# Kernel tuning notes

Measured on AMD Instinct MI355X. Metric: run time of the kernel, lower is better.

## Reference

```python
import jax, jax.numpy as jnp
import numpy as np
from jax import lax

D_MODEL = 512
N_BLOCKS = 8
VOCAB = 2048
MEL = 80
D_INNER = 2 * D_MODEL      # standard Mamba expand=2
STATE = 16                 # AudioConstants.MAMBA_STATE_DIM
DT_RANK = D_MODEL // 16    # 32
CONV_K = 4                 # causal depthwise conv kernel
B, T = 4, 2048


def setup_inputs() -> dict:
    key = jax.random.key(0)
    ks = jax.random.split(key, 16)
    s = 0.02
    nb = N_BLOCKS
    inp = {
        "feats": jax.random.normal(ks[0], (B, T, MEL), jnp.float32),
        "feat_lens": jax.random.randint(ks[1], (B,), 0, T, jnp.int32),
        # frontend
        "conv1_w": jax.random.normal(ks[2], (D_MODEL, MEL, 3), jnp.float32) * s,
        "conv1_b": jnp.zeros((D_MODEL,), jnp.float32),
        "conv2_w": jax.random.normal(ks[3], (D_MODEL, D_MODEL, 3), jnp.float32) * s,
        "conv2_b": jnp.zeros((D_MODEL,), jnp.float32),
        # stacked per-block Mamba params (leading dim = n_blocks)
        "norm_w": jnp.ones((nb, D_MODEL), jnp.float32),
        "in_proj_w": jax.random.normal(ks[4], (nb, D_MODEL, 2 * D_INNER), jnp.float32) * s,
        "dwconv_w": jax.random.normal(ks[5], (nb, D_INNER, CONV_K), jnp.float32) * s,
        "dwconv_b": jnp.zeros((nb, D_INNER), jnp.float32),
        "x_proj_w": jax.random.normal(ks[6], (nb, D_INNER, DT_RANK + 2 * STATE), jnp.float32) * s,
        "dt_proj_w": jax.random.normal(ks[7], (nb, DT_RANK, D_INNER), jnp.float32) * s,
        "dt_proj_b": jnp.full((nb, D_INNER), -4.6, jnp.float32),  # softplus(-4.6)~0.01
        "A_log": jnp.tile(jnp.log(jnp.arange(1, STATE + 1, dtype=jnp.float32))[None, None, :], (nb, D_INNER, 1)),
        "Dskip": jnp.ones((nb, D_INNER), jnp.float32),
        "out_proj_w": jax.random.normal(ks[8], (nb, D_INNER, D_MODEL), jnp.float32) * s,
        # CTC head
        "head_w": jax.random.normal(ks[9], (D_MODEL, VOCAB), jnp.float32) * s,
        "head_b": jnp.zeros((VOCAB,), jnp.float32),
    }
    return inp


def _conv1d(x, w, b, stride, pad):
    # x: (B, Cin, L), w: (Cout, Cin, K)
    y = lax.conv_general_dilated(x, w, (stride,), [(pad, pad)],
                                 dimension_numbers=("NCH", "OIH", "NCH"))
    return y + b[None, :, None]


def _mamba_layer(x, p):
    nw, ipw, cw, cb, xpw, dpw, dpb, alog, dsk, opw = p
    res = x
    # RMSNorm
    xn = x * lax.rsqrt(jnp.mean(x * x, axis=-1, keepdims=True) + 1e-5) * nw
    xz = xn @ ipw                                # (B, L, 2*di)
    xs, z = jnp.split(xz, 2, axis=-1)
    # causal depthwise conv over time
    xc = jnp.pad(xs.transpose(0, 2, 1), ((0, 0), (0, 0), (CONV_K - 1, 0)))
    xc = lax.conv_general_dilated(xc, cw[:, None, :], (1,), [(0, 0)],
                                  dimension_numbers=("NCH", "OIH", "NCH"),
                                  feature_group_count=D_INNER)
    xs = jax.nn.silu((xc + cb[None, :, None]).transpose(0, 2, 1))  # (B, L, di)
    # input-dependent SSM params
    xdb = xs @ xpw                               # (B, L, dt_rank + 2N)
    dt, Bm, Cm = jnp.split(xdb, [DT_RANK, DT_RANK + STATE], axis=-1)
    delta = jax.nn.softplus(dt @ dpw + dpb)      # (B, L, di)
    A = -jnp.exp(alog)                           # (di, N)
    dA = jnp.exp(delta[..., None] * A)           # (B, L, di, N)
    dBx = delta[..., None] * Bm[:, :, None, :] * xs[..., None]

    def step(h, inp):
        dA_t, dBx_t, C_t = inp                   # (B,di,N),(B,di,N),(B,N)
        h = dA_t * h + dBx_t
        y = jnp.einsum("bdn,bn->bd", h, C_t)
        return h, y

    h0 = jnp.zeros((x.shape[0], D_INNER, STATE), x.dtype)
    _, ys = lax.scan(step, h0, (dA.transpose(1, 0, 2, 3),
                                dBx.transpose(1, 0, 2, 3),
                                Cm.transpose(1, 0, 2)))
    y = ys.transpose(1, 0, 2) + xs * dsk          # (B, L, di)
    y = y * jax.nn.silu(z)
    return res + y @ opw, None


def reference(feats, feat_lens, conv1_w, conv1_b, conv2_w, conv2_b,
              norm_w, in_proj_w, dwconv_w, dwconv_b, x_proj_w,
              dt_proj_w, dt_proj_b, A_log, Dskip, out_proj_w,
              head_w, head_b):
    x = feats.transpose(0, 2, 1)                  # (B, 80, T)
    x = jax.nn.gelu(_conv1d(x, conv1_w, conv1_b, 2, 1), approximate=False)
    x = jax.nn.gelu(_conv1d(x, conv2_w, conv2_b, 2, 1), approximate=False)
    x = x.transpose(0, 2, 1)                      # (B, T/4, D)
    params = (norm_w, in_proj_w, dwconv_w, dwconv_b, x_proj_w,
              dt_proj_w, dt_proj_b, A_log, Dskip, out_proj_w)
    x, _ = lax.scan(_mamba_layer, x, params)
    logits = x @ head_w + head_b                  # (B, T/4, V)
    out_lens = jnp.maximum(feat_lens // 4, 1)
    return logits, out_lens
```

## Files before the change

kernel.cpp:

```cpp
#include <hip/hip_runtime.h>
#include <hip/hip_bf16.h>

#define DMODEL 512
#define NB 8
#define VOCABSZ 2048
#define MEL 80
#define DIN 1024
#define NSTATE 16
#define DTRANK 32
#define BATCH 4
#define TIN 2048
#define LL1 1024
#define LSEQ 512
#define MROWS (BATCH*LSEQ)
#define M1ROWS (BATCH*LL1)
#define NCHUNK 16
#define LCHUNK 32

typedef unsigned short u16;
typedef unsigned int   u32;
typedef __attribute__((ext_vector_type(8))) short short8;
typedef __attribute__((ext_vector_type(4))) float f32x4;

__device__ __forceinline__ float bf2f(u16 v) { return __uint_as_float(((u32)v) << 16); }
__device__ __forceinline__ u16 f2bf(float f) {
    u32 u = __float_as_uint(f);
    return (u16)((u + 0x7fffu + ((u >> 16) & 1u)) >> 16);
}
__device__ __forceinline__ float gelu_exact(float v) {
    return 0.5f * v * (1.0f + erff(v * 0.70710678118654752f));
}
__device__ __forceinline__ float silu_f(float v) { return v / (1.0f + __expf(-v)); }
__device__ __forceinline__ float softplus_f(float v) { return v > 20.f ? v : log1pf(__expf(v)); }

template<int WM, int WN, int MR, int NR, int EPI, int SPLITK>
__global__ __launch_bounds__(WM*WN*64) void gemm2_bf16(
    const u16* __restrict__ A, int lda,
    const u16* __restrict__ BT, int ldb,
    const float* __restrict__ bias,
    float* __restrict__ Cf, u16* __restrict__ Cb, int ldc,
    int K, int zstride)
{
    constexpr int BM = WM * MR * 16;
    constexpr int BN = WN * NR * 16;
    constexpr int NT = WM * WN * 64;
    constexpr int LA = (BM * 4) / NT;
    constexpr int LB = (BN * 4) / NT;
    __shared__ __align__(16) u16 As[2][BM * 32];
    __shared__ __align__(16) u16 Bs[2][BN * 32];
    const int tid = threadIdx.x;
    const int m0 = blockIdx.y * BM, n0 = blockIdx.x * BN;
    const int lane = tid & 63;
    const int wave = tid >> 6;
    const int wm = wave / WN, wn = wave % WN;
    const int lr = lane & 15, lk = lane >> 4;

    int kt0 = 0, kend = K;
    if (SPLITK > 1) {
        const int kb = K / SPLITK;
        kt0 = blockIdx.z * kb;
        kend = kt0 + kb;
        Cf += (size_t)blockIdx.z * zstride;
    }

    f32x4 acc[MR][NR];
#pragma unroll
    for (int m = 0; m < MR; ++m)
#pragma unroll
        for (int n = 0; n < NR; ++n) acc[m][n] = (f32x4){0.f, 0.f, 0.f, 0.f};

    auto stage = [&](int buf, int kt) {
#pragma unroll
        for (int c = 0; c < LA; ++c) {
            int idx = c * NT + tid;
            const u16* src = A + (size_t)(m0 + (idx >> 2)) * lda + kt + (idx & 3) * 8;
            __builtin_amdgcn_global_load_lds(
                (const __attribute__((address_space(1))) void*)src,
                (__attribute__((address_space(3))) void*)&As[buf][idx * 8], 16, 0, 0);
        }
#pragma unroll
        for (int c = 0; c < LB; ++c) {
            int idx = c * NT + tid;
            const u16* src = BT + (size_t)(n0 + (idx >> 2)) * ldb + kt + (idx & 3) * 8;
            __builtin_amdgcn_global_load_lds(
                (const __attribute__((address_space(1))) void*)src,
                (__attribute__((address_space(3))) void*)&Bs[buf][idx * 8], 16, 0, 0);
        }
    };

    stage(0, kt0);
    __syncthreads();
    int cur = 0;
    for (int kt = kt0; kt < kend; kt += 32) {
        if (kt + 32 < kend) stage(cur ^ 1, kt + 32);
        short8 a[MR], b[NR];
#pragma unroll
        for (int m = 0; m < MR; ++m)
            a[m] = *(const short8*)&As[cur][((wm * MR + m) * 16 + lr) * 32 + lk * 8];
#pragma unroll
        for (int n = 0; n < NR; ++n)
            b[n] = *(const short8*)&Bs[cur][((wn * NR + n) * 16 + lr) * 32 + lk * 8];
#pragma unroll
        for (int m = 0; m < MR; ++m)
#pragma unroll
            for (int n = 0; n < NR; ++n)
                acc[m][n] = __builtin_amdgcn_mfma_f32_16x16x32_bf16(a[m], b[n], acc[m][n], 0, 0, 0);
        __syncthreads();
        cur ^= 1;
    }

#pragma unroll
    for (int m = 0; m < MR; ++m) {
#pragma unroll
        for (int n = 0; n < NR; ++n) {
#pragma unroll
            for (int r = 0; r < 4; ++r) {
                const int row = m0 + (wm * MR + m) * 16 + lk * 4 + r;
                const int col = n0 + (wn * NR + n) * 16 + lr;
                float v = acc[m][n][r];
                if (EPI == 1)      v += bias[col];
                else if (EPI == 2) v = gelu_exact(v + bias[col]);
                else if (EPI == 3) v = softplus_f(v + bias[col]);
                else if (EPI == 4) v += Cf[(size_t)row * ldc + col];
                if (Cf) Cf[(size_t)row * ldc + col] = v;
                if (Cb) Cb[(size_t)row * ldc + col] = f2bf(v);
            }
        }
    }
}

__global__ __launch_bounds__(256) void tcast_k(const float* __restrict__ in, u16* __restrict__ out,
                                               int R, int C, size_t sin, size_t sout) {
    in  += (size_t)blockIdx.z * sin;
    out += (size_t)blockIdx.z * sout;
    __shared__ float s[32][33];
    const int tx = threadIdx.x & 31, ty = threadIdx.x >> 5;
    const int r0 = blockIdx.y * 32, c0 = blockIdx.x * 32;
#pragma unroll
    for (int i = 0; i < 4; ++i)
        s[ty + i * 8][tx] = in[(size_t)(r0 + ty + i * 8) * C + c0 + tx];
    __syncthreads();
#pragma unroll
    for (int i = 0; i < 4; ++i)
        out[(size_t)(c0 + ty + i * 8) * R + r0 + tx] = f2bf(s[tx][ty + i * 8]);
}

__global__ void castpad_k(const float* __restrict__ in, u16* __restrict__ out,
                          int rows, int cin, int cout, int instride,
                          size_t sin, size_t sout) {
    in  += (size_t)blockIdx.z * sin;
    out += (size_t)blockIdx.z * sout;
    int idx = blockIdx.x * 256 + threadIdx.x;
    if (idx >= rows * cout) return;
    int c = idx % cout, r = idx / cout;
    out[idx] = (c < cin) ? f2bf(in[(size_t)r * instride + c]) : (u16)0;
}

__global__ void im2col1_k(const float* __restrict__ feats, u16* __restrict__ out) {
    int idx = blockIdx.x * 256 + threadIdx.x;
    int c = idx & 255, m = idx >> 8;
    int l1 = m & (LL1 - 1), b = m >> 10;
    float v = 0.f;
    if (c < 240) {
        int ci = c / 3, kk = c - ci * 3;
        int t = 2 * l1 - 1 + kk;
        if (t >= 0 && t < TIN) v = feats[((size_t)b * TIN + t) * MEL + ci];
    }
    out[idx] = f2bf(v);
}

__global__ void im2col2_k(const float* __restrict__ y1, u16* __restrict__ out) {
    int idx = blockIdx.x * 256 + threadIdx.x;
    int c = idx % 1536, m = idx / 1536;
    int l = m & (LSEQ - 1), b = m >> 9;
    int ci = c / 3, kk = c - ci * 3;
    int t = 2 * l - 1 + kk;
    float v = (t >= 0 && t < LL1) ? y1[((size_t)b * LL1 + t) * 512 + ci] : 0.f;
    out[idx] = f2bf(v);
}

__global__ __launch_bounds__(256) void rmsnorm_k(const float* __restrict__ x,
                                                 const float* __restrict__ nw,
                                                 u16* __restrict__ xn) {
    int m = blockIdx.x;
    int tid = threadIdx.x;
    const float2 v = *reinterpret_cast<const float2*>(&x[(size_t)m * DMODEL + tid * 2]);
    float ss = v.x * v.x + v.y * v.y;
#pragma unroll
    for (int o = 32; o > 0; o >>= 1) ss += __shfl_down(ss, o);
    __shared__ float sred[4];
    __shared__ float sscale;
    if ((tid & 63) == 0) sred[tid >> 6] = ss;
    __syncthreads();
    if (tid == 0) {
        float tot = sred[0] + sred[1] + sred[2] + sred[3];
        sscale = rsqrtf(tot / 512.f + 1e-5f);
    }
    __syncthreads();
    float sc = sscale;
    u32 pack = (u32)f2bf(v.x * sc * nw[tid * 2]) | ((u32)f2bf(v.y * sc * nw[tid * 2 + 1]) << 16);
    *reinterpret_cast<u32*>(&xn[(size_t)m * DMODEL + tid * 2]) = pack;
}

__global__ __launch_bounds__(256) void dwconv_silu_k(const u16* __restrict__ xzb,
                                                     const float* __restrict__ cw,
                                                     const float* __restrict__ cb,
                                                     float* __restrict__ xs,
                                                     u16* __restrict__ xsb) {
    int d = blockIdx.x * 256 + threadIdx.x;
    int m = blockIdx.y;
    int l = m & (LSEQ - 1);
    int b = m >> 9;
    float acc = cb[d];
    const float4 w4 = *reinterpret_cast<const float4*>(&cw[d * 4]);
    const float wk[4] = {w4.x, w4.y, w4.z, w4.w};
#pragma unroll
    for (int k = 0; k < 4; k++) {
        int t = l - 3 + k;
        if (t >= 0) acc += wk[k] * bf2f(xzb[((size_t)(b * LSEQ + t)) * (2 * DIN) + d]);
    }
    float o = silu_f(acc);
    xs[(size_t)m * DIN + d] = o;
    xsb[(size_t)m * DIN + d] = f2bf(o);
}

__global__ void xreduce_k(const float* __restrict__ part, float* __restrict__ xdb,
                          u16* __restrict__ dtb) {
    int idx = blockIdx.x * 256 + threadIdx.x;
    float s = part[idx] + part[131072 + idx] + part[262144 + idx] + part[393216 + idx];
    xdb[idx] = s;
    int c = idx & 63, r = idx >> 6;
    if (c < 32) dtb[r * 32 + c] = f2bf(s);
}

template<int PASS>
__global__ __launch_bounds__(256) void scan_chunk_k(
    const u16* __restrict__ deltab, const float* __restrict__ xs,
    const float* __restrict__ xdb, const u16* __restrict__ xzb,
    const float* __restrict__ alog, const float* __restrict__ dsk,
    const float* __restrict__ hin,
    float* __restrict__ Pout, float* __restrict__ Qout,
    u16* __restrict__ yb)
{
    __shared__ float s_bc[LCHUNK * 32];
    __shared__ float s_dl[LCHUNK * 64];
    __shared__ float s_xs[LCHUNK * 64];
    __shared__ float s_z [PASS ? LCHUNK * 64 : 1];

    const int tid  = threadIdx.x;
    const int j    = tid & 3;
    const int dsub = tid >> 2;
    const int d0   = blockIdx.x * 64;
    const int c    = blockIdx.y;
    const int b    = blockIdx.z;
    const int d    = d0 + dsub;
    const size_t rbase = (size_t)b * LSEQ + c * LCHUNK;

    for (int idx = tid; idx < LCHUNK * 32; idx += 256) {
        int t = idx >> 5, cc = idx & 31;
        s_bc[idx] = xdb[(rbase + t) * 64 + 32 + cc];
    }
    for (int idx = tid; idx < LCHUNK * 64; idx += 256) {
        int t = idx >> 6, dd = idx & 63;
        s_dl[idx] = bf2f(deltab[(rbase + t) * DIN + d0 + dd]);
        s_xs[idx] = xs[(rbase + t) * DIN + d0 + dd];
        if (PASS) s_z[idx] = bf2f(xzb[(rbase + t) * (2 * DIN) + DIN + d0 + dd]);
    }
    __syncthreads();

    float a[4], h[4];
#pragma unroll
    for (int nj = 0; nj < 4; nj++)
        a[nj] = -__expf(alog[(size_t)d * NSTATE + j * 4 + nj]);

    const size_t chbase = ((size_t)(b * NCHUNK + c) * DIN + d) * NSTATE + j * 4;
    if (PASS) {
        const float4 h4 = *reinterpret_cast<const float4*>(&hin[chbase]);
        h[0] = h4.x; h[1] = h4.y; h[2] = h4.z; h[3] = h4.w;
    } else {
        h[0] = h[1] = h[2] = h[3] = 0.f;
    }
    const float dskv = PASS ? dsk[d] : 0.f;
    float sdl = 0.f;

    for (int t = 0; t < LCHUNK; t++) {
        const float dl = s_dl[t * 64 + dsub];
        const float xv = s_xs[t * 64 + dsub];
        const float dlx = dl * xv;
        if (!PASS) sdl += dl;
        float yv = 0.f;
#pragma unroll
        for (int nj = 0; nj < 4; nj++) {
            const float bn = s_bc[t * 32 + j * 4 + nj];
            const float dA = __expf(dl * a[nj]);
            h[nj] = fmaf(dA, h[nj], dlx * bn);
            if (PASS) {
                const float cn = s_bc[t * 32 + 16 + j * 4 + nj];
                yv = fmaf(h[nj], cn, yv);
            }
        }
        if (PASS) {
            yv += __shfl_xor(yv, 1);
            yv += __shfl_xor(yv, 2);
            if (j == 0) {
                const float zv = s_z[t * 64 + dsub];
                yb[(rbase + t) * DIN + d] = f2bf((yv + xv * dskv) * silu_f(zv));
            }
        }
    }

    if (!PASS) {
        float4 Pv, Qv;
        Pv.x = __expf(a[0] * sdl); Pv.y = __expf(a[1] * sdl);
        Pv.z = __expf(a[2] * sdl); Pv.w = __expf(a[3] * sdl);
        Qv.x = h[0]; Qv.y = h[1]; Qv.z = h[2]; Qv.w = h[3];
        *reinterpret_cast<float4*>(&Pout[chbase]) = Pv;
        *reinterpret_cast<float4*>(&Qout[chbase]) = Qv;
    }
}

__global__ __launch_bounds__(256) void scan_mid_k(const float* __restrict__ P,
                                                  float* __restrict__ Q) {
    const int tid = blockIdx.x * 256 + threadIdx.x;
    const int b  = tid >> 14;
    const int dn = tid & 16383;
    const size_t base = (size_t)b * (NCHUNK * DIN * NSTATE) + dn;
    float p[NCHUNK], q[NCHUNK];
#pragma unroll
    for (int c = 0; c < NCHUNK; c++) {
        p[c] = P[base + (size_t)c * (DIN * NSTATE)];
        q[c] = Q[base + (size_t)c * (DIN * NSTATE)];
    }
    float h = 0.f;
    Q[base] = 0.f;
#pragma unroll
    for (int c = 1; c < NCHUNK; c++) {
        h = fmaf(p[c - 1], h, q[c - 1]);
        Q[base + (size_t)c * (DIN * NSTATE)] = h;
    }
}

__global__ void lens_k(const int* __restrict__ feat_lens, float* __restrict__ out) {
    int b = threadIdx.x;
    if (b < BATCH) {
        int v = feat_lens[b] / 4;
        if (v < 1) v = 1;
        out[b] = (float)v;
    }
}

extern "C" void kernel_launch(void* const* d_in, const int* in_sizes, int n_in,
                              void* d_out, int out_size, void* d_ws, size_t ws_size,
                              hipStream_t stream)
{
    const float* feats = (const float*)d_in[0];
    const int*   flens = (const int*)  d_in[1];
    const float* c1w = (const float*)d_in[2];
    const float* c1b = (const float*)d_in[3];
    const float* c2w = (const float*)d_in[4];
    const float* c2b = (const float*)d_in[5];
    const float* nw  = (const float*)d_in[6];
    const float* ipw = (const float*)d_in[7];
    const float* cw  = (const float*)d_in[8];
    const float* cb  = (const float*)d_in[9];
    const float* xpw = (const float*)d_in[10];
    const float* dpw = (const float*)d_in[11];
    const float* dpb = (const float*)d_in[12];
    const float* alog= (const float*)d_in[13];
    const float* dskp= (const float*)d_in[14];
    const float* opw = (const float*)d_in[15];
    const float* hw  = (const float*)d_in[16];
    const float* hb  = (const float*)d_in[17];

    float* ws = (float*)d_ws;
    u16*  XZb   = (u16*)ws;
    float* X    = ws + 2097152;
    u16*  XN    = (u16*)(ws + 3145728);
    u16*  Xb    = (u16*)(ws + 3670016);
    float* XS   = ws + 4194304;
    u16*  XSb   = (u16*)(ws + 6291456);
    u16*  DELb  = (u16*)(ws + 7340032);
    float* XDB  = ws + 8388608;
    float* P    = ws + 8519680;
    u16*  dtb   = (u16*)(ws + 9568256);
    u16*  Yb    = (u16*)(ws + 9633792);
    float* XDBp = ws + 10682368;
    u16*  ipwT  = (u16*)(ws + 11206656);
    u16*  opwT  = (u16*)(ws + 11730944);
    u16*  hwT   = (u16*)(ws + 11993088);
    u16*  xpwT  = (u16*)(ws + 12517376);
    u16*  dpwT  = (u16*)(ws + 12779520);
    u16*  c1wb  = (u16*)(ws + 12910592);
    u16*  c2wb  = (u16*)(ws + 12976128);
    float* Y1   = XS;
    float* logits = (float*)d_out;
    float* Q    = logits;

    castpad_k<<<dim3(512, 1, 1), 256, 0, stream>>>(c1w, c1wb, 512, 240, 256, 240, 0, 0);
    castpad_k<<<dim3(3072, 1, 1), 256, 0, stream>>>(c2w, c2wb, 512, 1536, 1536, 1536, 0, 0);
    tcast_k<<<dim3(64, 16, 1), 256, 0, stream>>>(hw, hwT, 512, 2048, 0, 0);
    tcast_k<<<dim3(2, 32, 8), 256, 0, stream>>>(xpw, xpwT, 1024, 64, 65536, 65536);
    tcast_k<<<dim3(32, 1, 8), 256, 0, stream>>>(dpw, dpwT, 32, 1024, 32768, 32768);

    im2col1_k<<<4096, 256, 0, stream>>>(feats, XZb);
    gemm2_bf16<2, 2, 4, 2, 2, 1><<<dim3(8, 32), 256, 0, stream>>>(
        XZb, 256, c1wb, 256, c1b, Y1, nullptr, 512, 256, 0);
    im2col2_k<<<12288, 256, 0, stream>>>(Y1, XZb);
    gemm2_bf16<2, 2, 2, 2, 2, 1><<<dim3(8, 32), 256, 0, stream>>>(
        XZb, 1536, c2wb, 1536, c2b, X, nullptr, 512, 1536, 0);

    for (int blk = 0; blk < NB; ++blk) {
        tcast_k<<<dim3(64, 16, 1), 256, 0, stream>>>(ipw + (size_t)blk * 1048576, ipwT, 512, 2048, 0, 0);
        tcast_k<<<dim3(16, 32, 1), 256, 0, stream>>>(opw + (size_t)blk * 524288, opwT, 1024, 512, 0, 0);
        rmsnorm_k<<<MROWS, 256, 0, stream>>>(X, nw + blk * DMODEL, XN);
        gemm2_bf16<2, 2, 4, 2, 0, 1><<<dim3(32, 16), 256, 0, stream>>>(
            XN, 512, ipwT, 512, nullptr, nullptr, XZb, 2048, 512, 0);
        dwconv_silu_k<<<dim3(4, MROWS), 256, 0, stream>>>(
            XZb, cw + blk * DIN * 4, cb + blk * DIN, XS, XSb);
        gemm2_bf16<2, 2, 2, 2, 0, 4><<<dim3(1, 32, 4), 256, 0, stream>>>(
            XSb, 1024, xpwT + (size_t)blk * 65536, 1024, nullptr,
            XDBp, nullptr, 64, 1024, 131072);
        xreduce_k<<<512, 256, 0, stream>>>(XDBp, XDB, dtb);
        gemm2_bf16<2, 2, 4, 2, 3, 1><<<dim3(16, 16), 256, 0, stream>>>(
            dtb, 32, dpwT + (size_t)blk * 32768, 32, dpb + blk * DIN,
            nullptr, DELb, 1024, 32, 0);
        scan_chunk_k<0><<<dim3(16, NCHUNK, BATCH), 256, 0, stream>>>(
            DELb, XS, XDB, nullptr, alog + (size_t)blk * DIN * NSTATE,
            nullptr, nullptr, P, Q, nullptr);
        scan_mid_k<<<256, 256, 0, stream>>>(P, Q);
        scan_chunk_k<1><<<dim3(16, NCHUNK, BATCH), 256, 0, stream>>>(
            DELb, XS, XDB, XZb, alog + (size_t)blk * DIN * NSTATE,
            dskp + blk * DIN, Q, nullptr, nullptr, Yb);
        gemm2_bf16<2, 2, 2, 2, 4, 1><<<dim3(8, 32), 256, 0, stream>>>(
            Yb, 1024, opwT, 1024, nullptr, X, Xb, 512, 1024, 0);
    }

    gemm2_bf16<2, 2, 4, 2, 1, 1><<<dim3(32, 16), 256, 0, stream>>>(
        Xb, 512, hwT, 512, hb, logits, nullptr, 2048, 512, 0);
    lens_k<<<1, 64, 0, stream>>>(flens, logits + (size_t)MROWS * VOCABSZ);
}
```

Measured before the change: 884.7 us.

## Hoist weight casts, drop fp32 activations, fold chunk-carry scan into second pass

Moves the per-block in_proj and out_proj transpose-cast kernels out of the layer loop into one batched launch each. The conv1 output and the dwconv output are now stored only as bf16, which removes the fp32 XS buffer and its writes and reads. The xreduce kernel is vectorised with float4 loads and packed stores. The separate scan_mid kernel is removed; each second-pass scan block now rebuilds its carry-in state by walking the previous chunks' P/Q. This saves one launch per layer but adds redundant serial work that grows with the chunk index, and storing xs in bf16 lowers scan precision.

```diff
diff --git a/kernel.cpp b/kernel.cpp
--- a/kernel.cpp
+++ b/kernel.cpp
@@ -169,14 +169,13 @@
     out[idx] = f2bf(v);
 }
 
-__global__ void im2col2_k(const float* __restrict__ y1, u16* __restrict__ out) {
+__global__ void im2col2_k(const u16* __restrict__ y1b, u16* __restrict__ out) {
     int idx = blockIdx.x * 256 + threadIdx.x;
     int c = idx % 1536, m = idx / 1536;
     int l = m & (LSEQ - 1), b = m >> 9;
     int ci = c / 3, kk = c - ci * 3;
     int t = 2 * l - 1 + kk;
-    float v = (t >= 0 && t < LL1) ? y1[((size_t)b * LL1 + t) * 512 + ci] : 0.f;
-    out[idx] = f2bf(v);
+    out[idx] = (t >= 0 && t < LL1) ? y1b[((size_t)b * LL1 + t) * 512 + ci] : (u16)0;
 }
 
 __global__ __launch_bounds__(256) void rmsnorm_k(const float* __restrict__ x,
@@ -205,7 +204,6 @@
 __global__ __launch_bounds__(256) void dwconv_silu_k(const u16* __restrict__ xzb,
                                                      const float* __restrict__ cw,
                                                      const float* __restrict__ cb,
-                                                     float* __restrict__ xs,
                                                      u16* __restrict__ xsb) {
     int d = blockIdx.x * 256 + threadIdx.x;
     int m = blockIdx.y;
@@ -219,27 +217,37 @@
         int t = l - 3 + k;
         if (t >= 0) acc += wk[k] * bf2f(xzb[((size_t)(b * LSEQ + t)) * (2 * DIN) + d]);
     }
-    float o = silu_f(acc);
-    xs[(size_t)m * DIN + d] = o;
-    xsb[(size_t)m * DIN + d] = f2bf(o);
+    xsb[(size_t)m * DIN + d] = f2bf(silu_f(acc));
 }
 
 __global__ void xreduce_k(const float* __restrict__ part, float* __restrict__ xdb,
                           u16* __restrict__ dtb) {
-    int idx = blockIdx.x * 256 + threadIdx.x;
-    float s = part[idx] + part[131072 + idx] + part[262144 + idx] + part[393216 + idx];
-    xdb[idx] = s;
-    int c = idx & 63, r = idx >> 6;
-    if (c < 32) dtb[r * 32 + c] = f2bf(s);
+    int i4 = blockIdx.x * 256 + threadIdx.x;
+    const float4 p0 = *(const float4*)&part[i4 * 4];
+    const float4 p1 = *(const float4*)&part[131072 + i4 * 4];
+    const float4 p2 = *(const float4*)&part[262144 + i4 * 4];
+    const float4 p3 = *(const float4*)&part[393216 + i4 * 4];
+    float4 s;
+    s.x = p0.x + p1.x + p2.x + p3.x;
+    s.y = p0.y + p1.y + p2.y + p3.y;
+    s.z = p0.z + p1.z + p2.z + p3.z;
+    s.w = p0.w + p1.w + p2.w + p3.w;
+    *(float4*)&xdb[i4 * 4] = s;
+    int c4 = i4 & 15, r = i4 >> 4;
+    if (c4 < 8) {
+        u32 lo = (u32)f2bf(s.x) | ((u32)f2bf(s.y) << 16);
+        u32 hi = (u32)f2bf(s.z) | ((u32)f2bf(s.w) << 16);
+        *(u32*)&dtb[r * 32 + c4 * 4]     = lo;
+        *(u32*)&dtb[r * 32 + c4 * 4 + 2] = hi;
+    }
 }
 
 template<int PASS>
 __global__ __launch_bounds__(256) void scan_chunk_k(
-    const u16* __restrict__ deltab, const float* __restrict__ xs,
+    const u16* __restrict__ deltab, const u16* __restrict__ xsb,
     const float* __restrict__ xdb, const u16* __restrict__ xzb,
     const float* __restrict__ alog, const float* __restrict__ dsk,
-    const float* __restrict__ hin,
-    float* __restrict__ Pout, float* __restrict__ Qout,
+    float* __restrict__ P, float* __restrict__ Q,
     u16* __restrict__ yb)
 {
     __shared__ float s_bc[LCHUNK * 32];
@@ -263,7 +271,7 @@
     for (int idx = tid; idx < LCHUNK * 64; idx += 256) {
         int t = idx >> 6, dd = idx & 63;
         s_dl[idx] = bf2f(deltab[(rbase + t) * DIN + d0 + dd]);
-        s_xs[idx] = xs[(rbase + t) * DIN + d0 + dd];
+        s_xs[idx] = bf2f(xsb[(rbase + t) * DIN + d0 + dd]);
         if (PASS) s_z[idx] = bf2f(xzb[(rbase + t) * (2 * DIN) + DIN + d0 + dd]);
     }
     __syncthreads();
@@ -273,12 +281,19 @@
     for (int nj = 0; nj < 4; nj++)
         a[nj] = -__expf(alog[(size_t)d * NSTATE + j * 4 + nj]);
 
-    const size_t chbase = ((size_t)(b * NCHUNK + c) * DIN + d) * NSTATE + j * 4;
+    const size_t chstride = (size_t)DIN * NSTATE;
+    const size_t chcol = (size_t)d * NSTATE + j * 4;
+    h[0] = h[1] = h[2] = h[3] = 0.f;
     if (PASS) {
-        const float4 h4 = *reinterpret_cast<const float4*>(&hin[chbase]);
-        h[0] = h4.x; h[1] = h4.y; h[2] = h4.z; h[3] = h4.w;
-    } else {
-        h[0] = h[1] = h[2] = h[3] = 0.f;
+        for (int c2 = 0; c2 < c; ++c2) {
+            const size_t o = ((size_t)(b * NCHUNK + c2)) * chstride + chcol;
+            const float4 Pv = *(const float4*)&P[o];
+            const float4 Qv = *(const float4*)&Q[o];
+            h[0] = fmaf(Pv.x, h[0], Qv.x);
+            h[1] = fmaf(Pv.y, h[1], Qv.y);
+            h[2] = fmaf(Pv.z, h[2], Qv.z);
+            h[3] = fmaf(Pv.w, h[3], Qv.w);
+        }
     }
     const float dskv = PASS ? dsk[d] : 0.f;
     float sdl = 0.f;
@@ -310,33 +325,13 @@
     }
 
     if (!PASS) {
+        const size_t o = ((size_t)(b * NCHUNK + c)) * chstride + chcol;
         float4 Pv, Qv;
         Pv.x = __expf(a[0] * sdl); Pv.y = __expf(a[1] * sdl);
         Pv.z = __expf(a[2] * sdl); Pv.w = __expf(a[3] * sdl);
         Qv.x = h[0]; Qv.y = h[1]; Qv.z = h[2]; Qv.w = h[3];
-        *reinterpret_cast<float4*>(&Pout[chbase]) = Pv;
-        *reinterpret_cast<float4*>(&Qout[chbase]) = Qv;
-    }
-}
-
-__global__ __launch_bounds__(256) void scan_mid_k(const float* __restrict__ P,
-                                                  float* __restrict__ Q) {
-    const int tid = blockIdx.x * 256 + threadIdx.x;
-    const int b  = tid >> 14;
-    const int dn = tid & 16383;
-    const size_t base = (size_t)b * (NCHUNK * DIN * NSTATE) + dn;
-    float p[NCHUNK], q[NCHUNK];
-#pragma unroll
-    for (int c = 0; c < NCHUNK; c++) {
-        p[c] = P[base + (size_t)c * (DIN * NSTATE)];
-        q[c] = Q[base + (size_t)c * (DIN * NSTATE)];
-    }
-    float h = 0.f;
-    Q[base] = 0.f;
-#pragma unroll
-    for (int c = 1; c < NCHUNK; c++) {
-        h = fmaf(p[c - 1], h, q[c - 1]);
-        Q[base + (size_t)c * (DIN * NSTATE)] = h;
+        *(float4*)&P[o] = Pv;
+        *(float4*)&Q[o] = Qv;
     }
 }
 
@@ -373,66 +368,66 @@
     const float* hb  = (const float*)d_in[17];
 
     float* ws = (float*)d_ws;
-    u16*  XZb   = (u16*)ws;
-    float* X    = ws + 2097152;
-    u16*  XN    = (u16*)(ws + 3145728);
-    u16*  Xb    = (u16*)(ws + 3670016);
-    float* XS   = ws + 4194304;
-    u16*  XSb   = (u16*)(ws + 6291456);
-    u16*  DELb  = (u16*)(ws + 7340032);
-    float* XDB  = ws + 8388608;
-    float* P    = ws + 8519680;
-    u16*  dtb   = (u16*)(ws + 9568256);
-    u16*  Yb    = (u16*)(ws + 9633792);
-    float* XDBp = ws + 10682368;
-    u16*  ipwT  = (u16*)(ws + 11206656);
-    u16*  opwT  = (u16*)(ws + 11730944);
-    u16*  hwT   = (u16*)(ws + 11993088);
-    u16*  xpwT  = (u16*)(ws + 12517376);
-    u16*  dpwT  = (u16*)(ws + 12779520);
-    u16*  c1wb  = (u16*)(ws + 12910592);
-    u16*  c2wb  = (u16*)(ws + 12976128);
-    float* Y1   = XS;
+    u16*  XZb    = (u16*)ws;
+    float* X     = ws + 2097152;
+    u16*  XN     = (u16*)(ws + 3145728);
+    u16*  Xb     = (u16*)(ws + 3670016);
+    u16*  XSb    = (u16*)(ws + 4194304);
+    u16*  DELb   = (u16*)(ws + 5242880);
+    float* XDB   = ws + 6291456;
+    float* P     = ws + 6422528;
+    u16*  dtb    = (u16*)(ws + 7471104);
+    u16*  Yb     = (u16*)(ws + 7503872);
+    float* XDBp  = ws + 8552448;
+    u16*  ipwTa  = (u16*)(ws + 9076736);
+    u16*  opwTa  = (u16*)(ws + 13271040);
+    u16*  hwT    = (u16*)(ws + 15368192);
+    u16*  xpwT   = (u16*)(ws + 15892480);
+    u16*  dpwT   = (u16*)(ws + 16154624);
+    u16*  c1wb   = (u16*)(ws + 16285696);
+    u16*  c2wb   = (u16*)(ws + 16351232);
+    u16*  Y1b    = (u16*)(ws + 16744448);
     float* logits = (float*)d_out;
-    float* Q    = logits;
+    float* Q     = logits;
 
     castpad_k<<<dim3(512, 1, 1), 256, 0, stream>>>(c1w, c1wb, 512, 240, 256, 240, 0, 0);
     castpad_k<<<dim3(3072, 1, 1), 256, 0, stream>>>(c2w, c2wb, 512, 1536, 1536, 1536, 0, 0);
     tcast_k<<<dim3(64, 16, 1), 256, 0, stream>>>(hw, hwT, 512, 2048, 0, 0);
     tcast_k<<<dim3(2, 32, 8), 256, 0, stream>>>(xpw, xpwT, 1024, 64, 65536, 65536);
     tcast_k<<<dim3(32, 1, 8), 256, 0, stream>>>(dpw, dpwT, 32, 1024, 32768, 32768);
+    tcast_k<<<dim3(64, 16, 8), 256, 0, stream>>>(ipw, ipwTa, 512, 2048, 1048576, 1048576);
+    tcast_k<<<dim3(16, 32, 8), 256, 0, stream>>>(opw, opwTa, 1024, 512, 524288, 524288);
 
     im2col1_k<<<4096, 256, 0, stream>>>(feats, XZb);
     gemm2_bf16<2, 2, 4, 2, 2, 1><<<dim3(8, 32), 256, 0, stream>>>(
-        XZb, 256, c1wb, 256, c1b, Y1, nullptr, 512, 256, 0);
-    im2col2_k<<<12288, 256, 0, stream>>>(Y1, XZb);
+        XZb, 256, c1wb, 256, c1b, nullptr, Y1b, 512, 256, 0);
+    im2col2_k<<<12288, 256, 0, stream>>>(Y1b, XZb);
     gemm2_bf16<2, 2, 2, 2, 2, 1><<<dim3(8, 32), 256, 0, stream>>>(
         XZb, 1536, c2wb, 1536, c2b, X, nullptr, 512, 1536, 0);
 
     for (int blk = 0; blk < NB; ++blk) {
-        tcast_k<<<dim3(64, 16, 1), 256, 0, stream>>>(ipw + (size_t)blk * 1048576, ipwT, 512, 2048, 0, 0);
-        tcast_k<<<dim3(16, 32, 1), 256, 0, stream>>>(opw + (size_t)blk * 524288, opwT, 1024, 512, 0, 0);
         rmsnorm_k<<<MROWS, 256, 0, stream>>>(X, nw + blk * DMODEL, XN);
         gemm2_bf16<2, 2, 4, 2, 0, 1><<<dim3(32, 16), 256, 0, stream>>>(
-            XN, 512, ipwT, 512, nullptr, nullptr, XZb, 2048, 512, 0);
+            XN, 512, ipwTa + (size_t)blk * 1048576, 512, nullptr,
+            nullptr, XZb, 2048, 512, 0);
         dwconv_silu_k<<<dim3(4, MROWS), 256, 0, stream>>>(
-            XZb, cw + blk * DIN * 4, cb + blk * DIN, XS, XSb);
+            XZb, cw + blk * DIN * 4, cb + blk * DIN, XSb);
         gemm2_bf16<2, 2, 2, 2, 0, 4><<<dim3(1, 32, 4), 256, 0, stream>>>(
             XSb, 1024, xpwT + (size_t)blk * 65536, 1024, nullptr,
             XDBp, nullptr, 64, 1024, 131072);
-        xreduce_k<<<512, 256, 0, stream>>>(XDBp, XDB, dtb);
+        xreduce_k<<<128, 256, 0, stream>>>(XDBp, XDB, dtb);
         gemm2_bf16<2, 2, 4, 2, 3, 1><<<dim3(16, 16), 256, 0, stream>>>(
             dtb, 32, dpwT + (size_t)blk * 32768, 32, dpb + blk * DIN,
             nullptr, DELb, 1024, 32, 0);
         scan_chunk_k<0><<<dim3(16, NCHUNK, BATCH), 256, 0, stream>>>(
-            DELb, XS, XDB, nullptr, alog + (size_t)blk * DIN * NSTATE,
-            nullptr, nullptr, P, Q, nullptr);
-        scan_mid_k<<<256, 256, 0, stream>>>(P, Q);
+            DELb, XSb, XDB, nullptr, alog + (size_t)blk * DIN * NSTATE,
+            nullptr, P, Q, nullptr);
         scan_chunk_k<1><<<dim3(16, NCHUNK, BATCH), 256, 0, stream>>>(
-            DELb, XS, XDB, XZb, alog + (size_t)blk * DIN * NSTATE,
-            dskp + blk * DIN, Q, nullptr, nullptr, Yb);
+            DELb, XSb, XDB, XZb, alog + (size_t)blk * DIN * NSTATE,
+            dskp + blk * DIN, P, Q, Yb);
         gemm2_bf16<2, 2, 2, 2, 4, 1><<<dim3(8, 32), 256, 0, stream>>>(
-            Yb, 1024, opwT, 1024, nullptr, X, Xb, 512, 1024, 0);
+            Yb, 1024, opwTa + (size_t)blk * 524288, 1024, nullptr,
+            X, Xb, 512, 1024, 0);
     }
 
     gemm2_bf16<2, 2, 4, 2, 1, 1><<<dim3(32, 16), 256, 0, stream>>>(
```

Result: faster. 858.6 us (-2.9%).
